# Kernel tuning notes

Hardware: AMD Instinct MI355X
Metric: run time of the kernel (lower is better)

Reference implementation:

```python
import jax, jax.numpy as jnp
import numpy as np

K = 3          # kernel size
STRIDE = 1
PAD = 1
DIL = 1
BN_EPS = 1e-5


def _conv2d(x, w, b, stride=STRIDE, pad=PAD):
    out = jax.lax.conv_general_dilated(
        x, w, (stride, stride), [(pad, pad), (pad, pad)],
        dimension_numbers=("NCHW", "OIHW", "NCHW"))
    return out + b[None, :, None, None]


def _bilinear_sample(x, py, px):
    """Zero-padded bilinear sampling. x: [B,C,H,W]; py,px: [B,Ho,Wo] float coords."""
    B, C, H, W = x.shape
    y0 = jnp.floor(py)
    x0 = jnp.floor(px)
    wy1 = py - y0
    wx1 = px - x0
    x_flat = x.reshape(B, C, H * W)

    def gather(yi, xi, wgt):
        valid = (yi >= 0) & (yi <= H - 1) & (xi >= 0) & (xi <= W - 1)
        yc = jnp.clip(yi, 0, H - 1).astype(jnp.int32)
        xc = jnp.clip(xi, 0, W - 1).astype(jnp.int32)
        idx = (yc * W + xc).reshape(B, 1, -1)                      # [B,1,Ho*Wo]
        v = jnp.take_along_axis(x_flat, idx, axis=2)               # [B,C,Ho*Wo]
        v = v.reshape(B, C, py.shape[1], py.shape[2])
        return v * (wgt * valid)[:, None]

    return (gather(y0,     x0,     (1 - wy1) * (1 - wx1)) +
            gather(y0,     x0 + 1, (1 - wy1) * wx1) +
            gather(y0 + 1, x0,     wy1 * (1 - wx1)) +
            gather(y0 + 1, x0 + 1, wy1 * wx1))


def _forward(x, off_w, off_b, dc_w, dc_b, bn_gamma, bn_beta, bn_mean, bn_var):
    B, C, H, W = x.shape
    K2 = K * K
    om = _conv2d(x, off_w, off_b)                 # [B, 3*K2, H, W]
    offset = om[:, :2 * K2]                       # interleaved (dy, dx) per tap
    mask = jax.nn.sigmoid(om[:, 2 * K2:])         # [B, K2, H, W]

    # output pixel -> top-left input coordinate of the receptive field
    base_y = (jnp.arange(H) * STRIDE - PAD)[:, None]   # [H,1]
    base_x = (jnp.arange(W) * STRIDE - PAD)[None, :]   # [1,W]

    out = jnp.zeros((B, dc_w.shape[0], H, W), dtype=x.dtype)
    for k in range(K2):
        kh, kw = k // K, k % K
        py = base_y + kh * DIL + offset[:, 2 * k]      # [B,H,W]
        px = base_x + kw * DIL + offset[:, 2 * k + 1]  # [B,H,W]
        samp = _bilinear_sample(x, py, px) * mask[:, k][:, None]
        out = out + jnp.einsum('oc,bchw->bohw', dc_w[:, :, kh, kw], samp)
    out = out + dc_b[None, :, None, None]

    # BatchNorm (inference: running stats) + ReLU
    scale = bn_gamma / jnp.sqrt(bn_var + BN_EPS)
    out = out * scale[None, :, None, None] + (bn_beta - bn_mean * scale)[None, :, None, None]
    return jax.nn.relu(out)


def setup_inputs() -> dict:
    key = jax.random.key(0)
    ks = jax.random.split(key, 8)
    B, Cin, Cout, H, W = 8, 256, 256, 64, 64
    K2 = K * K
    x = jax.random.normal(ks[0], (B, Cin, H, W), dtype=jnp.float32)
    # NOTE: original init zeros the offset conv; we use small random weights so
    # offsets/masks are nontrivial and the bilinear path is exercised.
    off_w = jax.random.normal(ks[1], (3 * K2, Cin, K, K), dtype=jnp.float32) * 0.01
    off_b = jax.random.normal(ks[2], (3 * K2,), dtype=jnp.float32) * 0.01
    dc_w = jax.random.normal(ks[3], (Cout, Cin, K, K), dtype=jnp.float32) / np.sqrt(Cin * K2)
    dc_b = jax.random.normal(ks[4], (Cout,), dtype=jnp.float32) * 0.01
    bn_gamma = jnp.ones((Cout,), dtype=jnp.float32)
    bn_beta = jnp.zeros((Cout,), dtype=jnp.float32)
    bn_mean = jax.random.normal(ks[5], (Cout,), dtype=jnp.float32) * 0.1
    bn_var = jax.random.uniform(ks[6], (Cout,), dtype=jnp.float32) * 0.5 + 0.5
    return {"x": x, "off_w": off_w, "off_b": off_b, "dc_w": dc_w, "dc_b": dc_b,
            "bn_gamma": bn_gamma, "bn_beta": bn_beta,
            "bn_mean": bn_mean, "bn_var": bn_var}


def reference(x, off_w, off_b, dc_w, dc_b, bn_gamma, bn_beta, bn_mean, bn_var):
    return _forward(x, off_w, off_b, dc_w, dc_b, bn_gamma, bn_beta, bn_mean, bn_var)
```

## Files before the change

### kernel.cpp

```cpp
#include <hip/hip_runtime.h>
#include <hip/hip_bf16.h>
#include <hip/hip_fp16.h>
#include <cstdint>
#include <cstddef>

#define HH 64
#define WW 64
#define CIN 256
#define COUT 256
#define NB 8
#define HW (HH * WW)
#define BN_EPS 1e-5f

typedef __attribute__((ext_vector_type(8))) short s16x8;
typedef __attribute__((ext_vector_type(8))) unsigned short u16x8;
typedef __attribute__((ext_vector_type(4))) float f32x4;

static __device__ __forceinline__ float bf2f(unsigned short u) {
  unsigned int v = ((unsigned int)u) << 16;
  return __builtin_bit_cast(float, v);
}
static __device__ __forceinline__ unsigned short f2bf(float f) {
  __hip_bfloat16 h = __float2bfloat16(f);
  return __builtin_bit_cast(unsigned short, h);
}

__global__ __launch_bounds__(256) void k_tr(const float* __restrict__ x,
                                            unsigned short* __restrict__ xbf) {
  __shared__ float tile[64][65];
  int bid = blockIdx.x;
  int b = bid & 7;
  int r = bid >> 3;
  int ct = r & 3;
  int st = r >> 2;
  int lane = threadIdx.x & 63;
  int grp = threadIdx.x >> 6;
  int c0 = ct * 64, s0 = st * 64;
  const float* xb = x + (size_t)b * CIN * HW;
#pragma unroll
  for (int i = 0; i < 16; ++i) {
    int row = grp * 16 + i;
    tile[row][lane] = xb[(size_t)(c0 + row) * HW + s0 + lane];
  }
  __syncthreads();
  unsigned short* xo = xbf + (size_t)b * HW * CIN;
#pragma unroll
  for (int i = 0; i < 16; ++i) {
    int row = grp * 16 + i;
    xo[(size_t)(s0 + row) * CIN + c0 + lane] = f2bf(tile[lane][row]);
  }
}

__global__ __launch_bounds__(256) void k_wt(const float* __restrict__ dc_w,
                                            unsigned short* __restrict__ Wf) {
  int idx = blockIdx.x * 256 + threadIdx.x;
  if (idx >= 9 * 8 * 16 * 64 * 8) return;
  int j = idx & 7;
  int lane = (idx >> 3) & 63;
  int tile = (idx >> 9) & 15;
  int ks = (idx >> 13) & 7;
  int k = idx >> 16;
  int o = tile * 16 + (lane & 15);
  int c = ks * 32 + (lane >> 4) * 8 + j;
  Wf[idx] = f2bf(dc_w[((size_t)o * CIN + c) * 9 + k]);
}

__global__ __launch_bounds__(256) void k_owt(const float* __restrict__ off_w,
                                             unsigned short* __restrict__ OWf) {
  int idx = blockIdx.x * 256 + threadIdx.x;
  if (idx >= 9 * 8 * 2 * 64 * 8) return;
  int j = idx & 7;
  int lane = (idx >> 3) & 63;
  int kot = (idx >> 9) & 1;
  int ks = (idx >> 10) & 7;
  int t = idx >> 13;
  int ko = kot * 16 + (lane & 15);
  int c = ks * 32 + (lane >> 4) * 8 + j;
  unsigned short v = 0;
  if (ko < 27) v = f2bf(off_w[((size_t)ko * CIN + c) * 9 + t]);
  OWf[idx] = v;
}

__global__ void k_bn(const float* __restrict__ g, const float* __restrict__ be,
                     const float* __restrict__ m, const float* __restrict__ va,
                     const float* __restrict__ db, float* __restrict__ sc,
                     float* __restrict__ bi) {
  int o = threadIdx.x;
  float s = g[o] * rsqrtf(va[o] + BN_EPS);
  sc[o] = s;
  bi[o] = be[o] + (db[o] - m[o]) * s;
}

__global__ __launch_bounds__(512, 2) void k_main(
    const unsigned short* __restrict__ xbf, const unsigned short* __restrict__ OWf,
    const float* __restrict__ off_b, const unsigned short* __restrict__ Wf,
    const float* __restrict__ bnsc, const float* __restrict__ bnbi,
    float* __restrict__ out) {
  int bid = blockIdx.x;
  int b = bid & 7;
  int h = bid >> 3;
  int tid = threadIdx.x;
  int lane = tid & 63;
  int wave = tid >> 6;
  int l15 = lane & 15, l4 = lane >> 4;

  __shared__ __align__(16) unsigned short ubuf[66 * 256];
  __shared__ float om_lds[27][64];
  __shared__ unsigned short pre_offS[9][64][4];
  __shared__ __half pre_wH[9][64][4];

  const unsigned short* xb = xbf + (size_t)b * HW * CIN;

  if (tid < 64) {
    int r = (tid < 32) ? 0 : 65;
    int ch = tid & 31;
    u16x8 z = {0, 0, 0, 0, 0, 0, 0, 0};
    *(u16x8*)&ubuf[r * 256 + ch * 8] = z;
  }

  f32x4 acc_oc[2];
  acc_oc[0] = (f32x4){0.f, 0.f, 0.f, 0.f};
  acc_oc[1] = (f32x4){0.f, 0.f, 0.f, 0.f};
  int wavepx = (wave & 3) * 16;

  for (int kh = 0; kh < 3; ++kh) {
    int y = h + kh - 1;
    if (y < 0 || y >= HH) continue;
    __syncthreads();
    const unsigned short* src = xb + (size_t)y * WW * CIN;
#pragma unroll
    for (int i = 0; i < 4; ++i) {
      int e8 = i * 512 + tid;
      int px = e8 >> 5;
      int ch = e8 & 31;
      u16x8 v = *(const u16x8*)(src + e8 * 8);
      *(u16x8*)&ubuf[(px + 1) * 256 + ((ch ^ ((px + 1) & 7)) * 8)] = v;
    }
    __syncthreads();
    if (wave < 4) {
#pragma unroll
      for (int kw = 0; kw < 3; ++kw) {
        int prow = wavepx + l15 + kw;
        int rs = prow & 7;
        const unsigned short* Atap =
            OWf + ((size_t)(kh * 3 + kw) * 8) * 1024 + lane * 8;
#pragma unroll
        for (int ks = 0; ks < 8; ++ks) {
          s16x8 bfrag = *(const s16x8*)&ubuf[prow * 256 + (((ks * 4 + l4) ^ rs) * 8)];
#pragma unroll
          for (int kot = 0; kot < 2; ++kot) {
            s16x8 afrag = *(const s16x8*)(Atap + ks * 1024 + kot * 512);
            acc_oc[kot] = __builtin_amdgcn_mfma_f32_16x16x32_bf16(afrag, bfrag,
                                                                  acc_oc[kot], 0, 0, 0);
          }
        }
      }
    }
  }
  if (wave < 4) {
#pragma unroll
    for (int kot = 0; kot < 2; ++kot) {
#pragma unroll
      for (int j = 0; j < 4; ++j) {
        int ko = kot * 16 + l4 * 4 + j;
        if (ko < 27) om_lds[ko][wavepx + l15] = acc_oc[kot][j];
      }
    }
  }
  __syncthreads();

  for (int item = tid; item < 9 * 64; item += 512) {
    int k = item >> 6;
    int w = item & 63;
    int kh = k / 3, kw = k % 3;
    float offy = om_lds[2 * k][w] + off_b[2 * k];
    float offx = om_lds[2 * k + 1][w] + off_b[2 * k + 1];
    float mk = om_lds[18 + k][w] + off_b[18 + k];
    mk = 1.0f / (1.0f + expf(-mk));
    float py = (float)(h - 1 + kh) + offy;
    float px = (float)(w - 1 + kw) + offx;
    float fy0 = floorf(py), fx0 = floorf(px);
    float wy1 = py - fy0, wx1 = px - fx0;
    int y0 = (int)fy0, x0 = (int)fx0;
    int y1 = y0 + 1, x1 = x0 + 1;
    bool vy0 = (y0 >= 0) && (y0 <= HH - 1);
    bool vy1 = (y1 >= 0) && (y1 <= HH - 1);
    bool vx0 = (x0 >= 0) && (x0 <= WW - 1);
    bool vx1 = (x1 >= 0) && (x1 <= WW - 1);
    int y0c = min(max(y0, 0), HH - 1), y1c = min(max(y1, 0), HH - 1);
    int x0c = min(max(x0, 0), WW - 1), x1c = min(max(x1, 0), WW - 1);
    pre_wH[k][w][0] =
        __float2half((1.f - wy1) * (1.f - wx1) * mk * ((vy0 && vx0) ? 1.f : 0.f));
    pre_wH[k][w][1] = __float2half((1.f - wy1) * wx1 * mk * ((vy0 && vx1) ? 1.f : 0.f));
    pre_wH[k][w][2] = __float2half(wy1 * (1.f - wx1) * mk * ((vy1 && vx0) ? 1.f : 0.f));
    pre_wH[k][w][3] = __float2half(wy1 * wx1 * mk * ((vy1 && vx1) ? 1.f : 0.f));
    pre_offS[k][w][0] = (unsigned short)(y0c * WW + x0c);
    pre_offS[k][w][1] = (unsigned short)(y0c * WW + x1c);
    pre_offS[k][w][2] = (unsigned short)(y1c * WW + x0c);
    pre_offS[k][w][3] = (unsigned short)(y1c * WW + x1c);
  }

  unsigned short(*S)[256] = (unsigned short(*)[256])ubuf;
  f32x4 acc[2][4];
#pragma unroll
  for (int i = 0; i < 2; ++i)
#pragma unroll
    for (int j = 0; j < 4; ++j) acc[i][j] = (f32x4){0.f, 0.f, 0.f, 0.f};

  int pswz = lane & 7;
  int o_base = wave * 32;
  int hv = lane >> 5;
  int chunk = lane & 31;

  for (int k = 0; k < 9; ++k) {
    __syncthreads();
    {
#pragma unroll
      for (int pp = 0; pp < 4; ++pp) {
        int px = wave * 8 + pp * 2 + hv;
        int i0 = ((int)pre_offS[k][px][0]) << 8;
        int i1 = ((int)pre_offS[k][px][1]) << 8;
        int i2 = ((int)pre_offS[k][px][2]) << 8;
        int i3 = ((int)pre_offS[k][px][3]) << 8;
        float w0 = __half2float(pre_wH[k][px][0]);
        float w1 = __half2float(pre_wH[k][px][1]);
        float w2 = __half2float(pre_wH[k][px][2]);
        float w3 = __half2float(pre_wH[k][px][3]);
        u16x8 v0 = *(const u16x8*)(xb + i0 + chunk * 8);
        u16x8 v1 = *(const u16x8*)(xb + i1 + chunk * 8);
        u16x8 v2 = *(const u16x8*)(xb + i2 + chunk * 8);
        u16x8 v3 = *(const u16x8*)(xb + i3 + chunk * 8);
        u16x8 r;
#pragma unroll
        for (int j = 0; j < 8; ++j) {
          float s = w0 * bf2f(v0[j]) + w1 * bf2f(v1[j]) + w2 * bf2f(v2[j]) +
                    w3 * bf2f(v3[j]);
          r[j] = f2bf(s);
        }
        int phys = chunk ^ (px & 7);
        *(u16x8*)&S[px][phys * 8] = r;
      }
    }
    __syncthreads();
    const unsigned short* Wa = Wf + (size_t)k * 65536 + (wave * 2) * 512 + lane * 8;
#pragma unroll
    for (int ks = 0; ks < 8; ++ks) {
      s16x8 a[2], bf[4];
#pragma unroll
      for (int ot = 0; ot < 2; ++ot)
        a[ot] = *(const s16x8*)(Wa + ks * 8192 + ot * 512);
#pragma unroll
      for (int pt = 0; pt < 4; ++pt) {
        int slot = (ks * 4 + l4) ^ pswz;
        bf[pt] = *(const s16x8*)&S[pt * 16 + l15][slot * 8];
      }
#pragma unroll
      for (int ot = 0; ot < 2; ++ot)
#pragma unroll
        for (int pt = 0; pt < 4; ++pt)
          acc[ot][pt] = __builtin_amdgcn_mfma_f32_16x16x32_bf16(a[ot], bf[pt],
                                                                acc[ot][pt], 0, 0, 0);
    }
  }

#pragma unroll
  for (int ot = 0; ot < 2; ++ot) {
#pragma unroll
    for (int j = 0; j < 4; ++j) {
      int o = o_base + ot * 16 + l4 * 4 + j;
      float sc = bnsc[o], bi = bnbi[o];
      float* ob = out + (((size_t)b * COUT + o) * HH + h) * WW;
#pragma unroll
      for (int pt = 0; pt < 4; ++pt) {
        ob[pt * 16 + l15] = fmaxf(fmaf(acc[ot][pt][j], sc, bi), 0.f);
      }
    }
  }
}

extern "C" void kernel_launch(void* const* d_in, const int* in_sizes, int n_in,
                              void* d_out, int out_size, void* d_ws, size_t ws_size,
                              hipStream_t stream) {
  const float* x = (const float*)d_in[0];
  const float* off_w = (const float*)d_in[1];
  const float* off_b = (const float*)d_in[2];
  const float* dc_w = (const float*)d_in[3];
  const float* dc_b = (const float*)d_in[4];
  const float* bn_gamma = (const float*)d_in[5];
  const float* bn_beta = (const float*)d_in[6];
  const float* bn_mean = (const float*)d_in[7];
  const float* bn_var = (const float*)d_in[8];
  float* out = (float*)d_out;

  char* ws = (char*)d_ws;
  unsigned short* xbf = (unsigned short*)ws;
  ws += (size_t)NB * HW * CIN * sizeof(unsigned short);
  unsigned short* Wf = (unsigned short*)ws;
  ws += (size_t)9 * 8 * 16 * 64 * 8 * sizeof(unsigned short);
  unsigned short* OWf = (unsigned short*)ws;
  ws += (size_t)9 * 8 * 2 * 64 * 8 * sizeof(unsigned short);
  float* bnsc = (float*)ws;
  ws += 256 * sizeof(float);
  float* bnbi = (float*)ws;

  k_tr<<<NB * 64 * 4, 256, 0, stream>>>(x, xbf);
  k_wt<<<(9 * 8 * 16 * 64 * 8 + 255) / 256, 256, 0, stream>>>(dc_w, Wf);
  k_owt<<<(9 * 8 * 2 * 64 * 8 + 255) / 256, 256, 0, stream>>>(off_w, OWf);
  k_bn<<<1, 256, 0, stream>>>(bn_gamma, bn_beta, bn_mean, bn_var, dc_b, bnsc, bnbi);
  k_main<<<NB * HH, 512, 0, stream>>>(xbf, OWf, off_b, Wf, bnsc, bnbi, out);
}
```

Baseline: 116.1 us.

## Stage a 3-row input window in LDS for deformable bilinear gathers

Loads three input rows (bf16, channel-last) into a 96KB LDS window and precomputes LDS indices for bilinear taps that fall inside it. Taps outside the window fall back to the old global gathers. The window is rolled forward at taps 3 and 6. It also vectorises the bilinear blend with packed FMAs and a packed bf16 convert, and drops the 2-blocks-per-CU launch bound. The aim is to replace repeated global/L2 gathers with LDS reads, at the cost of much larger LDS use, lower occupancy, and extra barriers.

```diff
diff --git a/kernel.cpp b/kernel.cpp
--- a/kernel.cpp
+++ b/kernel.cpp
@@ -15,6 +15,8 @@
 typedef __attribute__((ext_vector_type(8))) short s16x8;
 typedef __attribute__((ext_vector_type(8))) unsigned short u16x8;
 typedef __attribute__((ext_vector_type(4))) float f32x4;
+typedef __attribute__((ext_vector_type(2))) float f32x2;
+typedef __attribute__((ext_vector_type(4))) unsigned int u32x4;
 
 static __device__ __forceinline__ float bf2f(unsigned short u) {
   unsigned int v = ((unsigned int)u) << 16;
@@ -23,6 +25,9 @@
 static __device__ __forceinline__ unsigned short f2bf(float f) {
   __hip_bfloat16 h = __float2bfloat16(f);
   return __builtin_bit_cast(unsigned short, h);
+}
+static __device__ __forceinline__ int iclamp(int v, int lo, int hi) {
+  return min(max(v, lo), hi);
 }
 
 __global__ __launch_bounds__(256) void k_tr(const float* __restrict__ x,
@@ -91,7 +96,7 @@
   bi[o] = be[o] + (db[o] - m[o]) * s;
 }
 
-__global__ __launch_bounds__(512, 2) void k_main(
+__global__ __launch_bounds__(512) void k_main(
     const unsigned short* __restrict__ xbf, const unsigned short* __restrict__ OWf,
     const float* __restrict__ off_b, const unsigned short* __restrict__ Wf,
     const float* __restrict__ bnsc, const float* __restrict__ bnbi,
@@ -104,18 +109,20 @@
   int wave = tid >> 6;
   int l15 = lane & 15, l4 = lane >> 4;
 
+  __shared__ __align__(16) unsigned short win[3 * 64 * 256];
   __shared__ __align__(16) unsigned short ubuf[66 * 256];
-  __shared__ float om_lds[27][64];
   __shared__ unsigned short pre_offS[9][64][4];
+  __shared__ unsigned short pre_lds[9][64][4];
   __shared__ __half pre_wH[9][64][4];
+  float(*om_lds)[64] = (float(*)[64])win;
 
   const unsigned short* xb = xbf + (size_t)b * HW * CIN;
 
   if (tid < 64) {
-    int r = (tid < 32) ? 0 : 65;
+    int rr = (tid < 32) ? 0 : 65;
     int ch = tid & 31;
     u16x8 z = {0, 0, 0, 0, 0, 0, 0, 0};
-    *(u16x8*)&ubuf[r * 256 + ch * 8] = z;
+    *(u16x8*)&ubuf[rr * 256 + ch * 8] = z;
   }
 
   f32x4 acc_oc[2];
@@ -187,8 +194,8 @@
     bool vy1 = (y1 >= 0) && (y1 <= HH - 1);
     bool vx0 = (x0 >= 0) && (x0 <= WW - 1);
     bool vx1 = (x1 >= 0) && (x1 <= WW - 1);
-    int y0c = min(max(y0, 0), HH - 1), y1c = min(max(y1, 0), HH - 1);
-    int x0c = min(max(x0, 0), WW - 1), x1c = min(max(x1, 0), WW - 1);
+    int y0c = iclamp(y0, 0, HH - 1), y1c = iclamp(y1, 0, HH - 1);
+    int x0c = iclamp(x0, 0, WW - 1), x1c = iclamp(x1, 0, WW - 1);
     pre_wH[k][w][0] =
         __float2half((1.f - wy1) * (1.f - wx1) * mk * ((vy0 && vx0) ? 1.f : 0.f));
     pre_wH[k][w][1] = __float2half((1.f - wy1) * wx1 * mk * ((vy0 && vx1) ? 1.f : 0.f));
@@ -198,7 +205,36 @@
     pre_offS[k][w][1] = (unsigned short)(y0c * WW + x1c);
     pre_offS[k][w][2] = (unsigned short)(y1c * WW + x0c);
     pre_offS[k][w][3] = (unsigned short)(y1c * WW + x1c);
-  }
+    int r0 = iclamp(h - 2 + kh, 0, HH - 1);
+    int r1 = iclamp(h - 1 + kh, 0, HH - 1);
+    int r2 = iclamp(h + kh, 0, HH - 1);
+    int i0 = (y0c == r0) ? 0 : (y0c == r1) ? 1 : (y0c == r2) ? 2 : -1;
+    int i1 = (y1c == r0) ? 0 : (y1c == r1) ? 1 : (y1c == r2) ? 2 : -1;
+    if (i0 >= 0 && i1 >= 0) {
+      int s0 = (kh + i0) % 3, s1 = (kh + i1) % 3;
+      pre_lds[k][w][0] = (unsigned short)(s0 * 64 + x0c);
+      pre_lds[k][w][1] = (unsigned short)(s0 * 64 + x1c);
+      pre_lds[k][w][2] = (unsigned short)(s1 * 64 + x0c);
+      pre_lds[k][w][3] = (unsigned short)(s1 * 64 + x1c);
+    } else {
+      pre_lds[k][w][0] = 0xFFFF;
+    }
+  }
+  __syncthreads();
+
+  {
+#pragma unroll
+    for (int s = 0; s < 3; ++s) {
+      int y = iclamp(h - 2 + s, 0, HH - 1);
+      const unsigned short* src = xb + (size_t)y * WW * CIN;
+#pragma unroll
+      for (int i = 0; i < 4; ++i) {
+        int idx = i * 512 + tid;
+        *(u16x8*)&win[s * 16384 + idx * 8] = *(const u16x8*)(src + idx * 8);
+      }
+    }
+  }
+  __syncthreads();
 
   unsigned short(*S)[256] = (unsigned short(*)[256])ubuf;
   f32x4 acc[2][4];
@@ -207,39 +243,73 @@
 #pragma unroll
     for (int j = 0; j < 4; ++j) acc[i][j] = (f32x4){0.f, 0.f, 0.f, 0.f};
 
-  int pswz = lane & 7;
   int o_base = wave * 32;
   int hv = lane >> 5;
   int chunk = lane & 31;
 
   for (int k = 0; k < 9; ++k) {
+    if (k == 3 || k == 6) {
+      __syncthreads();
+      int g_ = k / 3;
+      int y = iclamp(h + g_, 0, HH - 1);
+      int s = (g_ + 2) % 3;
+      const unsigned short* src = xb + (size_t)y * WW * CIN;
+#pragma unroll
+      for (int i = 0; i < 4; ++i) {
+        int idx = i * 512 + tid;
+        *(u16x8*)&win[s * 16384 + idx * 8] = *(const u16x8*)(src + idx * 8);
+      }
+    }
     __syncthreads();
-    {
-#pragma unroll
-      for (int pp = 0; pp < 4; ++pp) {
-        int px = wave * 8 + pp * 2 + hv;
-        int i0 = ((int)pre_offS[k][px][0]) << 8;
-        int i1 = ((int)pre_offS[k][px][1]) << 8;
-        int i2 = ((int)pre_offS[k][px][2]) << 8;
-        int i3 = ((int)pre_offS[k][px][3]) << 8;
-        float w0 = __half2float(pre_wH[k][px][0]);
-        float w1 = __half2float(pre_wH[k][px][1]);
-        float w2 = __half2float(pre_wH[k][px][2]);
-        float w3 = __half2float(pre_wH[k][px][3]);
-        u16x8 v0 = *(const u16x8*)(xb + i0 + chunk * 8);
-        u16x8 v1 = *(const u16x8*)(xb + i1 + chunk * 8);
-        u16x8 v2 = *(const u16x8*)(xb + i2 + chunk * 8);
-        u16x8 v3 = *(const u16x8*)(xb + i3 + chunk * 8);
-        u16x8 r;
-#pragma unroll
-        for (int j = 0; j < 8; ++j) {
-          float s = w0 * bf2f(v0[j]) + w1 * bf2f(v1[j]) + w2 * bf2f(v2[j]) +
-                    w3 * bf2f(v3[j]);
-          r[j] = f2bf(s);
-        }
-        int phys = chunk ^ (px & 7);
-        *(u16x8*)&S[px][phys * 8] = r;
-      }
+#pragma unroll
+    for (int pp = 0; pp < 4; ++pp) {
+      int pl = wave * 8 + pp * 2 + hv;
+      u32x4 m0, m1, m2, m3;
+      unsigned short c0 = pre_lds[k][pl][0];
+      if (c0 != 0xFFFF) {
+        unsigned short c1 = pre_lds[k][pl][1];
+        unsigned short c2 = pre_lds[k][pl][2];
+        unsigned short c3 = pre_lds[k][pl][3];
+        m0 = __builtin_bit_cast(u32x4, *(const u16x8*)&win[(int)c0 * 256 + chunk * 8]);
+        m1 = __builtin_bit_cast(u32x4, *(const u16x8*)&win[(int)c1 * 256 + chunk * 8]);
+        m2 = __builtin_bit_cast(u32x4, *(const u16x8*)&win[(int)c2 * 256 + chunk * 8]);
+        m3 = __builtin_bit_cast(u32x4, *(const u16x8*)&win[(int)c3 * 256 + chunk * 8]);
+      } else {
+        m0 = __builtin_bit_cast(
+            u32x4, *(const u16x8*)(xb + (((int)pre_offS[k][pl][0]) << 8) + chunk * 8));
+        m1 = __builtin_bit_cast(
+            u32x4, *(const u16x8*)(xb + (((int)pre_offS[k][pl][1]) << 8) + chunk * 8));
+        m2 = __builtin_bit_cast(
+            u32x4, *(const u16x8*)(xb + (((int)pre_offS[k][pl][2]) << 8) + chunk * 8));
+        m3 = __builtin_bit_cast(
+            u32x4, *(const u16x8*)(xb + (((int)pre_offS[k][pl][3]) << 8) + chunk * 8));
+      }
+      float w0 = __half2float(pre_wH[k][pl][0]);
+      float w1 = __half2float(pre_wH[k][pl][1]);
+      float w2 = __half2float(pre_wH[k][pl][2]);
+      float w3 = __half2float(pre_wH[k][pl][3]);
+      f32x2 w0p = {w0, w0}, w1p = {w1, w1}, w2p = {w2, w2}, w3p = {w3, w3};
+      u32x4 ro;
+#pragma unroll
+      for (int s = 0; s < 4; ++s) {
+        f32x2 t0 = {bf2f((unsigned short)(m0[s] & 0xffffu)),
+                    __builtin_bit_cast(float, m0[s] & 0xffff0000u)};
+        f32x2 t1 = {bf2f((unsigned short)(m1[s] & 0xffffu)),
+                    __builtin_bit_cast(float, m1[s] & 0xffff0000u)};
+        f32x2 t2 = {bf2f((unsigned short)(m2[s] & 0xffffu)),
+                    __builtin_bit_cast(float, m2[s] & 0xffff0000u)};
+        f32x2 t3 = {bf2f((unsigned short)(m3[s] & 0xffffu)),
+                    __builtin_bit_cast(float, m3[s] & 0xffff0000u)};
+        f32x2 a2 = t0 * w0p;
+        a2 = __builtin_elementwise_fma(t1, w1p, a2);
+        a2 = __builtin_elementwise_fma(t2, w2p, a2);
+        a2 = __builtin_elementwise_fma(t3, w3p, a2);
+        unsigned int o;
+        asm("v_cvt_pk_bf16_f32 %0, %1, %2" : "=v"(o) : "v"(a2[0]), "v"(a2[1]));
+        ro[s] = o;
+      }
+      int phys = chunk ^ (pl & 7);
+      *(u16x8*)&S[pl][phys * 8] = __builtin_bit_cast(u16x8, ro);
     }
     __syncthreads();
     const unsigned short* Wa = Wf + (size_t)k * 65536 + (wave * 2) * 512 + lane * 8;
@@ -251,8 +321,9 @@
         a[ot] = *(const s16x8*)(Wa + ks * 8192 + ot * 512);
 #pragma unroll
       for (int pt = 0; pt < 4; ++pt) {
-        int slot = (ks * 4 + l4) ^ pswz;
-        bf[pt] = *(const s16x8*)&S[pt * 16 + l15][slot * 8];
+        int pl = pt * 16 + l15;
+        int slot = (ks * 4 + l4) ^ (pl & 7);
+        bf[pt] = *(const s16x8*)&S[pl][slot * 8];
       }
 #pragma unroll
       for (int ot = 0; ot < 2; ++ot)
```

Result: slower. 121.8 us (+4.9%).
